# Kernel optimization log

Measured on AMD Instinct MI355X. Metric: run time of the kernel, lower is better.

The kernel has to match this reference:

```python
import jax, jax.numpy as jnp
import numpy as np


def _conv(x, w, b, stride=1):
    # NCHW conv, 3x3 kernel, padding=1
    y = jax.lax.conv_general_dilated(
        x, w, (stride, stride), [(1, 1), (1, 1)],
        dimension_numbers=("NCHW", "OIHW", "NCHW"))
    return y + b[None, :, None, None]


def setup_inputs() -> dict:
    key = jax.random.key(0)
    ks = jax.random.split(key, 13)
    s = 0.05
    d = jnp.float32
    return {
        "x": jax.random.normal(ks[0], (1, 3, 512, 512), d),
        "low0_w": jax.random.normal(ks[1], (64, 3, 3, 3), d) * s,
        "low0_b": jax.random.normal(ks[2], (64,), d) * s,
        "ll_rh_w": jax.random.normal(ks[3], (4, 61, 61, 3, 3), d) * s,
        "ll_rh_b": jax.random.normal(ks[4], (4, 61), d) * s,
        "ll_lh_w": jax.random.normal(ks[5], (4, 3, 3, 3, 3), d) * s,
        "ll_lh_b": jax.random.normal(ks[6], (4, 3), d) * s,
        "hl0_w": jax.random.normal(ks[7], (64, 61, 3, 3), d) * s,
        "hl0_b": jax.random.normal(ks[8], (64,), d) * s,
        "hl_w": jax.random.normal(ks[9], (3, 64, 64, 3, 3), d) * s,
        "hl_b": jax.random.normal(ks[10], (3, 64), d) * s,
        "lin_w": jax.random.normal(ks[11], (30, 64), d) * s,
        "lin_b": jax.random.normal(ks[12], (30,), d) * s,
    }


def reference(x, low0_w, low0_b, ll_rh_w, ll_rh_b, ll_lh_w, ll_lh_b,
              hl0_w, hl0_b, hl_w, hl_b, lin_w, lin_b):
    # ---- low-level path: 64-channel full-resolution features ----
    I = _conv(x, low0_w, low0_b)  # (b,64,H,W)
    for i in range(ll_rh_w.shape[0]):
        rh = jax.nn.relu(_conv(I[:, :61], ll_rh_w[i], ll_rh_b[i]))
        lh = jnp.tanh(_conv(I[:, 61:], ll_lh_w[i], ll_lh_b[i]))
        I = jnp.concatenate([rh, lh], axis=1)
    # ---- high-level path: predicts 30 params -> 3x10 color transform ----
    h = _conv(I[:, :61], hl0_w, hl0_b)
    for i in range(hl_w.shape[0]):
        h = jax.nn.relu(_conv(h, hl_w[i], hl_b[i], stride=2))
        h = jax.lax.reduce_window(h, -jnp.inf, jax.lax.max,
                                  (1, 1, 2, 2), (1, 1, 2, 2), "VALID")
    g = h.mean(axis=(2, 3))            # (b,64) global average pool
    Wp = g @ lin_w.T + lin_b           # (b,30)
    Wm = Wp.reshape(3, 10)             # batch=1, matches torch reshape
    # ---- vectorized Tform: per-pixel quadratic feature expansion ----
    I3 = I[:, 61:]                     # (b,3,H,W)
    r, gc, bc = I3[:, 0], I3[:, 1], I3[:, 2]
    feats = jnp.stack([r * r, r * gc, r * bc, r,
                       gc * gc, gc * bc, gc,
                       bc * bc, bc, jnp.ones_like(r)], axis=1)  # (b,10,H,W)
    return jnp.einsum("ok,bkhw->bohw", Wm, feats)  # (b,3,H,W)
```

## Files before the change

### kernel.cpp

```cpp
#include <hip/hip_runtime.h>
#include <cstdint>

typedef _Float16 half8 __attribute__((ext_vector_type(8)));
typedef float f32x4 __attribute__((ext_vector_type(4)));

#define HW_ (512*512)

__global__ __launch_bounds__(256) void wtrans_k(
    const float* __restrict__ rh_w, const float* __restrict__ hl0_w,
    const float* __restrict__ hl_w, _Float16* __restrict__ wt,
    _Float16* __restrict__ zg)
{
    if (blockIdx.x == 0 && threadIdx.x < 32) zg[threadIdx.x] = (_Float16)0.f;
    int t = blockIdx.x * 256 + threadIdx.x;
    if (t >= 8 * 4608) return;
    int layer = t / 4608;
    int r = t - layer * 4608;
    int lane = r & 63, ci = r >> 6;
    int m = ci & 3, kk = (ci >> 2) & 1, s = ci >> 3;
    int o = m * 16 + (lane & 15);
    int cb = kk * 32 + ((lane >> 4) & 3) * 8;
    const float* w; int O, CIN;
    if (layer < 4)      { w = rh_w + (size_t)layer * 61 * 61 * 9; O = 61; CIN = 61; }
    else if (layer == 4){ w = hl0_w;                              O = 64; CIN = 61; }
    else                { w = hl_w + (size_t)(layer - 5) * 64 * 64 * 9; O = 64; CIN = 64; }
    half8 v;
    #pragma unroll
    for (int j = 0; j < 8; ++j) {
        int c = cb + j;
        float f = (o < O && c < CIN) ? w[((size_t)o * CIN + c) * 9 + s] : 0.f;
        v[j] = (_Float16)f;
    }
    *(half8*)(wt + (size_t)layer * 36864 + (size_t)r * 8) = v;
}

__global__ __launch_bounds__(256)
void low0_k(const float* __restrict__ x, const float* __restrict__ w,
            const float* __restrict__ bias, _Float16* __restrict__ M,
            float* __restrict__ L)
{
    __shared__ float tile[3 * 324];
    const int tx = threadIdx.x & 15, ty = threadIdx.x >> 4;
    const int bx = blockIdx.x, by = blockIdx.y, z = blockIdx.z;
    const int ox = bx * 16 + tx, oy = by * 16 + ty;
    const int ix0 = bx * 16 - 1, iy0 = by * 16 - 1;

    for (int i = threadIdx.x; i < 3 * 324; i += 256) {
        int c = i / 324, p = i - c * 324;
        int iy = p / 18, ix = p - iy * 18;
        int gy = iy0 + iy, gx = ix0 + ix;
        float v = 0.f;
        if ((unsigned)gy < 512u && (unsigned)gx < 512u)
            v = x[(size_t)c * HW_ + (size_t)gy * 512 + gx];
        tile[i] = v;
    }
    __syncthreads();

    float p9[3][9];
    #pragma unroll
    for (int c = 0; c < 3; ++c)
        #pragma unroll
        for (int dy = 0; dy < 3; ++dy)
            #pragma unroll
            for (int dx = 0; dx < 3; ++dx)
                p9[c][dy * 3 + dx] = tile[c * 324 + (ty + dy) * 18 + tx + dx];

    float acc[16];
    #pragma unroll
    for (int o = 0; o < 16; ++o) {
        int oc = z * 16 + o;
        float a = bias[oc];
        const float* wo = w + (size_t)oc * 27;
        #pragma unroll
        for (int c = 0; c < 3; ++c)
            #pragma unroll
            for (int k = 0; k < 9; ++k)
                a = fmaf(p9[c][k], wo[c * 9 + k], a);
        acc[o] = a;
    }

    const size_t pix = (size_t)oy * 512 + ox;
    half8 h0, h1;
    #pragma unroll
    for (int o = 0; o < 8; ++o) { h0[o] = (_Float16)acc[o]; h1[o] = (_Float16)acc[8 + o]; }
    _Float16* orow = M + pix * 64 + z * 16;
    *(half8*)(orow)     = h0;
    *(half8*)(orow + 8) = h1;
    if (z == 3) {
        #pragma unroll
        for (int o = 13; o < 16; ++o)
            L[(size_t)(o - 13) * HW_ + pix] = acc[o];
    }
}

template<int O, int ACT, int DOLH>
__global__ __launch_bounds__(256, 3)
void conv_mfma_k(const _Float16* __restrict__ in, const _Float16* __restrict__ wt,
                 const float* __restrict__ bias, _Float16* __restrict__ out,
                 const float* __restrict__ L_in, const float* __restrict__ lhw,
                 const float* __restrict__ lhb, float* __restrict__ L_out,
                 const _Float16* __restrict__ zg)
{
    __shared__ _Float16 __attribute__((aligned(16))) in_t[2816 * 8];
    __shared__ float lh_t[3 * 324];
    const int tid = threadIdx.x;
    const int l = tid & 63, wv = tid >> 6;
    const int px = l & 15, g = l >> 4;
    const int bx = blockIdx.x, by = blockIdx.y;
    const int iy0 = by * 16 - 1, ix0 = bx * 16 - 1;

    #pragma unroll
    for (int k = 0; k < 11; ++k) {
        int i = tid + (k << 8);
        int p = i >> 3, jl = i & 7;
        int iy = p / 18, ix = p - iy * 18;
        int gy = iy0 + iy, gx = ix0 + ix;
        int j = jl ^ (p & 7);
        const _Float16* src =
            (p < 324 && (unsigned)gy < 512u && (unsigned)gx < 512u)
                ? in + ((size_t)gy * 512 + gx) * 64 + j * 8 : zg;
        __builtin_amdgcn_global_load_lds(
            (const __attribute__((address_space(1))) void*)src,
            (__attribute__((address_space(3))) void*)(in_t + (size_t)(tid - l + (k << 8)) * 8),
            16, 0, 0);
    }
    if (DOLH) {
        for (int i = tid; i < 3 * 324; i += 256) {
            int c = i / 324, p = i - c * 324;
            int iy = p / 18, ix = p - iy * 18;
            int gy = iy0 + iy, gx = ix0 + ix;
            float v = 0.f;
            if ((unsigned)gy < 512u && (unsigned)gx < 512u)
                v = L_in[(size_t)c * HW_ + (size_t)gy * 512 + gx];
            lh_t[i] = v;
        }
    }
    __syncthreads();

    float bs[4][4];
    #pragma unroll
    for (int m = 0; m < 4; ++m)
        #pragma unroll
        for (int r = 0; r < 4; ++r) {
            int o = m * 16 + g * 4 + r;
            bs[m][r] = (o < O) ? bias[o] : 0.f;
        }

    f32x4 acc[4][4];
    #pragma unroll
    for (int m = 0; m < 4; ++m)
        #pragma unroll
        for (int f = 0; f < 4; ++f) acc[m][f] = (f32x4){0.f, 0.f, 0.f, 0.f};

    const _Float16* wb = wt + (size_t)l * 8;
    half8 aA[8], aB[8];
    #pragma unroll
    for (int q = 0; q < 8; ++q) aA[q] = *(const half8*)(wb + q * 512);

    #pragma unroll
    for (int s = 0; s < 9; ++s) {
        asm volatile("" ::: "memory");
        const half8* ac = (s & 1) ? aB : aA;
        half8*       an = (s & 1) ? aA : aB;
        if (s < 8) {
            #pragma unroll
            for (int q = 0; q < 8; ++q)
                an[q] = *(const half8*)(wb + ((s + 1) * 8 + q) * 512);
        }
        const int dy = s / 3, dx = s - dy * 3;
        #pragma unroll
        for (int f = 0; f < 4; ++f) {
            int ipix = (4 * wv + f + dy) * 18 + px + dx;
            int rb = ipix * 64, sw = (ipix & 7) << 3;
            #pragma unroll
            for (int kk = 0; kk < 2; ++kk) {
                half8 b = *(const half8*)&in_t[rb + ((kk * 32 + g * 8) ^ sw)];
                #pragma unroll
                for (int m = 0; m < 4; ++m)
                    acc[m][f] = __builtin_amdgcn_mfma_f32_16x16x32_f16(
                        ac[kk * 4 + m], b, acc[m][f], 0, 0, 0);
            }
        }
    }

    if (DOLH) {
        const int tx = tid & 15, ty = tid >> 4;
        const size_t pix = (size_t)(by * 16 + ty) * 512 + bx * 16 + tx;
        #pragma unroll
        for (int oc = 0; oc < 3; ++oc) {
            float a = lhb[oc];
            #pragma unroll
            for (int c = 0; c < 3; ++c)
                #pragma unroll
                for (int t9 = 0; t9 < 9; ++t9) {
                    int dy = t9 / 3, dx = t9 - dy * 3;
                    a = fmaf(lh_t[c * 324 + (ty + dy) * 18 + tx + dx],
                             lhw[(oc * 3 + c) * 9 + t9], a);
                }
            L_out[(size_t)oc * HW_ + pix] = tanhf(a);
        }
    }

    __syncthreads();
    #pragma unroll
    for (int f = 0; f < 4; ++f) {
        const int p = (4 * wv + f) * 16 + px;
        const int sw = p & 7;
        #pragma unroll
        for (int m = 0; m < 4; ++m) {
            union { _Float16 h[4]; uint2 u; } pk;
            #pragma unroll
            for (int r = 0; r < 4; ++r) {
                int o = m * 16 + g * 4 + r;
                float v = acc[m][f][r] + bs[m][r];
                if (ACT) v = fmaxf(v, 0.f);
                pk.h[r] = (o < O) ? (_Float16)v : (_Float16)0.f;
            }
            int chunk = (m * 2 + (g >> 1)) ^ sw;
            *(uint2*)&in_t[p * 64 + chunk * 8 + (g & 1) * 4] = pk.u;
        }
    }
    __syncthreads();
    #pragma unroll
    for (int k = 0; k < 8; ++k) {
        int q = (k << 8) + tid;
        int p = q >> 3, jc = q & 7;
        half8 v = *(const half8*)&in_t[p * 64 + ((jc ^ (p & 7)) * 8)];
        int row = p >> 4, col = p & 15;
        _Float16* dst = out + (((size_t)(by * 16 + row) * 512) + bx * 16 + col) * 64 + jc * 8;
        *(half8*)dst = v;
    }
}

template<int FP32OUT>
__global__ __launch_bounds__(256, 3)
void conv_s2_pool_k(const _Float16* __restrict__ in, int Hin,
                    const _Float16* __restrict__ wt,
                    const float* __restrict__ bias, void* __restrict__ outv,
                    const _Float16* __restrict__ zg)
{
    const int Hp = Hin >> 2;
    __shared__ _Float16 __attribute__((aligned(16))) in_t[2560 * 8];
    const int tid = threadIdx.x;
    const int l = tid & 63, wv = tid >> 6;
    const int n = l & 15, g = l >> 4;
    const int bx = blockIdx.x, by = blockIdx.y;
    const int iy0 = by * 16 - 1, ix0 = bx * 16 - 1;

    #pragma unroll
    for (int k = 0; k < 10; ++k) {
        int i = tid + (k << 8);
        int p = i >> 3, jl = i & 7;
        int iy = p / 17, ix = p - iy * 17;
        int gy = iy0 + iy, gx = ix0 + ix;
        int j = jl ^ (p & 7);
        const _Float16* src =
            (p < 289 && (unsigned)gy < (unsigned)Hin && (unsigned)gx < (unsigned)Hin)
                ? in + ((size_t)gy * Hin + gx) * 64 + j * 8 : zg;
        __builtin_amdgcn_global_load_lds(
            (const __attribute__((address_space(1))) void*)src,
            (__attribute__((address_space(3))) void*)(in_t + (size_t)(tid - l + (k << 8)) * 8),
            16, 0, 0);
    }
    __syncthreads();

    float bs[4];
    #pragma unroll
    for (int r = 0; r < 4; ++r) bs[r] = bias[wv * 16 + g * 4 + r];

    f32x4 acc[4];
    #pragma unroll
    for (int f = 0; f < 4; ++f) acc[f] = (f32x4){0.f, 0.f, 0.f, 0.f};

    const int py_lo = n >> 3, pxc = n & 7;
    #pragma unroll
    for (int s = 0; s < 9; ++s) {
        const int dy = s / 3, dx = s - dy * 3;
        half8 a[2];
        #pragma unroll
        for (int kk = 0; kk < 2; ++kk)
            a[kk] = *(const half8*)(wt + (size_t)(s * 8 + kk * 4 + wv) * 512 + l * 8);
        #pragma unroll
        for (int f = 0; f < 4; ++f) {
            int py = 2 * f + py_lo;
            int ipix = (2 * py + dy) * 17 + 2 * pxc + dx;
            int rb = ipix * 64, sw = (ipix & 7) << 3;
            #pragma unroll
            for (int kk = 0; kk < 2; ++kk) {
                half8 b = *(const half8*)&in_t[rb + ((kk * 32 + g * 8) ^ sw)];
                acc[f] = __builtin_amdgcn_mfma_f32_16x16x32_f16(a[kk], b, acc[f], 0, 0, 0);
            }
        }
    }

    #pragma unroll
    for (int f = 0; f < 4; ++f)
        #pragma unroll
        for (int r = 0; r < 4; ++r) {
            float v = fmaxf(acc[f][r] + bs[r], 0.f);
            v = fmaxf(v, __shfl_xor(v, 1));
            v = fmaxf(v, __shfl_xor(v, 8));
            if ((l & 9) == 0) {
                int o = wv * 16 + g * 4 + r;
                size_t pp = ((size_t)(by * 4 + f) * Hp + bx * 4 + (n >> 1)) * 64 + o;
                if (FP32OUT) ((float*)outv)[pp] = v;
                else         ((_Float16*)outv)[pp] = (_Float16)v;
            }
        }
}

__global__ void meanlin_k(const float* __restrict__ h,
                          const float* __restrict__ lw,
                          const float* __restrict__ lb,
                          float* __restrict__ wm)
{
    __shared__ float g[64];
    int t = threadIdx.x;
    if (t < 64) {
        float s = 0.f;
        for (int p = 0; p < 64; ++p) s += h[p * 64 + t];
        g[t] = s * (1.f / 64.f);
    }
    __syncthreads();
    if (t < 30) {
        float s = lb[t];
        for (int c = 0; c < 64; ++c) s = fmaf(g[c], lw[t * 64 + c], s);
        wm[t] = s;
    }
}

__global__ __launch_bounds__(256)
void final_k(const float* __restrict__ I3, const float* __restrict__ wm,
             float* __restrict__ out)
{
    __shared__ float W[30];
    if (threadIdx.x < 30) W[threadIdx.x] = wm[threadIdx.x];
    __syncthreads();
    const int HW = 512 * 512;
    for (int i = blockIdx.x * blockDim.x + threadIdx.x; i < HW;
         i += gridDim.x * blockDim.x) {
        float r = I3[i], g = I3[HW + i], b = I3[2 * HW + i];
        float f[10] = { r * r, r * g, r * b, r, g * g, g * b, g, b * b, b, 1.f };
        #pragma unroll
        for (int o = 0; o < 3; ++o) {
            float s = 0.f;
            #pragma unroll
            for (int k = 0; k < 10; ++k) s = fmaf(W[o * 10 + k], f[k], s);
            out[(size_t)o * HW + i] = s;
        }
    }
}

extern "C" void kernel_launch(void* const* d_in, const int* in_sizes, int n_in,
                              void* d_out, int out_size, void* d_ws, size_t ws_size,
                              hipStream_t stream)
{
    const float* x      = (const float*)d_in[0];
    const float* low0_w = (const float*)d_in[1];
    const float* low0_b = (const float*)d_in[2];
    const float* rh_w   = (const float*)d_in[3];
    const float* rh_b   = (const float*)d_in[4];
    const float* lh_w   = (const float*)d_in[5];
    const float* lh_b   = (const float*)d_in[6];
    const float* hl0_w  = (const float*)d_in[7];
    const float* hl0_b  = (const float*)d_in[8];
    const float* hl_w   = (const float*)d_in[9];
    const float* hl_b   = (const float*)d_in[10];
    const float* lin_w  = (const float*)d_in[11];
    const float* lin_b  = (const float*)d_in[12];
    float* out = (float*)d_out;

    const size_t HW = 512 * 512;
    _Float16* M0 = (_Float16*)d_ws;
    _Float16* M1 = M0 + (size_t)64 * HW;
    _Float16* P0 = M1 + (size_t)64 * HW;
    _Float16* P1 = P0 + (size_t)16384 * 64;
    _Float16* WT = P1 + (size_t)1024 * 64;
    _Float16* ZG = WT + (size_t)8 * 36864;
    float*    P2 = (float*)(ZG + 32);
    float*    L0 = P2 + 64 * 64;
    float*    L1 = L0 + (size_t)3 * HW;
    float*    WM = L1 + (size_t)3 * HW;

    dim3 blk(256);
    dim3 g512(32, 32, 1);

    wtrans_k<<<dim3(144), blk, 0, stream>>>(rh_w, hl0_w, hl_w, WT, ZG);

    low0_k<<<dim3(32, 32, 4), blk, 0, stream>>>(x, low0_w, low0_b, M0, L0);

    _Float16* cur = M0; _Float16* nxt = M1;
    float* Lc = L0; float* Ln = L1;
    for (int i = 0; i < 4; ++i) {
        conv_mfma_k<61, 1, 1><<<g512, blk, 0, stream>>>(
            cur, WT + (size_t)i * 36864, rh_b + i * 61, nxt,
            Lc, lh_w + (size_t)i * 81, lh_b + i * 3, Ln, ZG);
        _Float16* t = cur; cur = nxt; nxt = t;
        float* tl = Lc; Lc = Ln; Ln = tl;
    }

    conv_mfma_k<64, 0, 0><<<g512, blk, 0, stream>>>(
        cur, WT + (size_t)4 * 36864, hl0_b, nxt,
        nullptr, nullptr, nullptr, nullptr, ZG);

    conv_s2_pool_k<0><<<dim3(32, 32), blk, 0, stream>>>(
        nxt, 512, WT + (size_t)5 * 36864, hl_b, (void*)P0, ZG);
    conv_s2_pool_k<0><<<dim3(8, 8), blk, 0, stream>>>(
        P0, 128, WT + (size_t)6 * 36864, hl_b + 64, (void*)P1, ZG);
    conv_s2_pool_k<1><<<dim3(2, 2), blk, 0, stream>>>(
        P1, 32, WT + (size_t)7 * 36864, hl_b + 128, (void*)P2, ZG);

    meanlin_k<<<dim3(1), dim3(64), 0, stream>>>(P2, lin_w, lin_b, WM);

    final_k<<<dim3(2048), blk, 0, stream>>>(Lc, WM, out);
}
```

Measured before the change: 259.7 us.

## Stage conv weights through double-buffered LDS via async global_load_lds

```diff
diff --git a/kernel.cpp b/kernel.cpp
--- a/kernel.cpp
+++ b/kernel.cpp
@@ -94,15 +94,16 @@
 }
 
 template<int O, int ACT, int DOLH>
-__global__ __launch_bounds__(256, 3)
+__global__ __launch_bounds__(256, 2)
 void conv_mfma_k(const _Float16* __restrict__ in, const _Float16* __restrict__ wt,
                  const float* __restrict__ bias, _Float16* __restrict__ out,
                  const float* __restrict__ L_in, const float* __restrict__ lhw,
                  const float* __restrict__ lhb, float* __restrict__ L_out,
                  const _Float16* __restrict__ zg)
 {
-    __shared__ _Float16 __attribute__((aligned(16))) in_t[2816 * 8];
-    __shared__ float lh_t[3 * 324];
+    __shared__ _Float16 __attribute__((aligned(16))) in_t[2592 * 8];
+    __shared__ _Float16 __attribute__((aligned(16))) wbuf[2][4096];
+    __shared__ float lh_t[DOLH ? 3 * 324 : 4];
     const int tid = threadIdx.x;
     const int l = tid & 63, wv = tid >> 6;
     const int px = l & 15, g = l >> 4;
@@ -112,16 +113,25 @@
     #pragma unroll
     for (int k = 0; k < 11; ++k) {
         int i = tid + (k << 8);
-        int p = i >> 3, jl = i & 7;
-        int iy = p / 18, ix = p - iy * 18;
-        int gy = iy0 + iy, gx = ix0 + ix;
-        int j = jl ^ (p & 7);
-        const _Float16* src =
-            (p < 324 && (unsigned)gy < 512u && (unsigned)gx < 512u)
+        if (i < 2592) {
+            int p = i >> 3, jl = i & 7;
+            int iy = p / 18, ix = p - iy * 18;
+            int gy = iy0 + iy, gx = ix0 + ix;
+            int j = jl ^ (p & 7);
+            const _Float16* src = ((unsigned)gy < 512u && (unsigned)gx < 512u)
                 ? in + ((size_t)gy * 512 + gx) * 64 + j * 8 : zg;
+            __builtin_amdgcn_global_load_lds(
+                (const __attribute__((address_space(1))) void*)src,
+                (__attribute__((address_space(3))) void*)(in_t + (size_t)(i - l) * 8),
+                16, 0, 0);
+        }
+    }
+    #pragma unroll
+    for (int it = 0; it < 2; ++it) {
+        int ci = (it << 8) + tid;
         __builtin_amdgcn_global_load_lds(
-            (const __attribute__((address_space(1))) void*)src,
-            (__attribute__((address_space(3))) void*)(in_t + (size_t)(tid - l + (k << 8)) * 8),
+            (const __attribute__((address_space(1))) void*)(wt + ci * 8),
+            (__attribute__((address_space(3))) void*)(wbuf[0] + (size_t)(ci - l) * 8),
             16, 0, 0);
     }
     if (DOLH) {
@@ -152,21 +162,24 @@
         #pragma unroll
         for (int f = 0; f < 4; ++f) acc[m][f] = (f32x4){0.f, 0.f, 0.f, 0.f};
 
-    const _Float16* wb = wt + (size_t)l * 8;
-    half8 aA[8], aB[8];
-    #pragma unroll
-    for (int q = 0; q < 8; ++q) aA[q] = *(const half8*)(wb + q * 512);
-
     #pragma unroll
     for (int s = 0; s < 9; ++s) {
-        asm volatile("" ::: "memory");
-        const half8* ac = (s & 1) ? aB : aA;
-        half8*       an = (s & 1) ? aA : aB;
         if (s < 8) {
             #pragma unroll
-            for (int q = 0; q < 8; ++q)
-                an[q] = *(const half8*)(wb + ((s + 1) * 8 + q) * 512);
-        }
+            for (int it = 0; it < 2; ++it) {
+                int ci = (it << 8) + tid;
+                __builtin_amdgcn_global_load_lds(
+                    (const __attribute__((address_space(1))) void*)(wt + ((s + 1) << 12) + ci * 8),
+                    (__attribute__((address_space(3))) void*)(wbuf[(s + 1) & 1] + (size_t)(ci - l) * 8),
+                    16, 0, 0);
+            }
+        }
+        const _Float16* wb = wbuf[s & 1];
+        half8 a[8];
+        #pragma unroll
+        for (int q = 0; q < 8; ++q)
+            a[q] = *(const half8*)(wb + (q << 9) + l * 8);
+
         const int dy = s / 3, dx = s - dy * 3;
         #pragma unroll
         for (int f = 0; f < 4; ++f) {
@@ -178,9 +191,10 @@
                 #pragma unroll
                 for (int m = 0; m < 4; ++m)
                     acc[m][f] = __builtin_amdgcn_mfma_f32_16x16x32_f16(
-                        ac[kk * 4 + m], b, acc[m][f], 0, 0, 0);
-            }
-        }
+                        a[kk * 4 + m], b, acc[m][f], 0, 0, 0);
+            }
+        }
+        __syncthreads();
     }
 
     if (DOLH) {
@@ -201,7 +215,6 @@
         }
     }
 
-    __syncthreads();
     #pragma unroll
     for (int f = 0; f < 4; ++f) {
         const int p = (4 * wv + f) * 16 + px;
@@ -240,7 +253,8 @@
                     const _Float16* __restrict__ zg)
 {
     const int Hp = Hin >> 2;
-    __shared__ _Float16 __attribute__((aligned(16))) in_t[2560 * 8];
+    __shared__ _Float16 __attribute__((aligned(16))) in_t[2312 * 8];
+    __shared__ _Float16 __attribute__((aligned(16))) wbuf[2][4096];
     const int tid = threadIdx.x;
     const int l = tid & 63, wv = tid >> 6;
     const int n = l & 15, g = l >> 4;
@@ -250,16 +264,26 @@
     #pragma unroll
     for (int k = 0; k < 10; ++k) {
         int i = tid + (k << 8);
-        int p = i >> 3, jl = i & 7;
-        int iy = p / 17, ix = p - iy * 17;
-        int gy = iy0 + iy, gx = ix0 + ix;
-        int j = jl ^ (p & 7);
-        const _Float16* src =
-            (p < 289 && (unsigned)gy < (unsigned)Hin && (unsigned)gx < (unsigned)Hin)
-                ? in + ((size_t)gy * Hin + gx) * 64 + j * 8 : zg;
+        if (i < 2312) {
+            int p = i >> 3, jl = i & 7;
+            int iy = p / 17, ix = p - iy * 17;
+            int gy = iy0 + iy, gx = ix0 + ix;
+            int j = jl ^ (p & 7);
+            const _Float16* src =
+                ((unsigned)gy < (unsigned)Hin && (unsigned)gx < (unsigned)Hin)
+                    ? in + ((size_t)gy * Hin + gx) * 64 + j * 8 : zg;
+            __builtin_amdgcn_global_load_lds(
+                (const __attribute__((address_space(1))) void*)src,
+                (__attribute__((address_space(3))) void*)(in_t + (size_t)(i - l) * 8),
+                16, 0, 0);
+        }
+    }
+    #pragma unroll
+    for (int it = 0; it < 2; ++it) {
+        int ci = (it << 8) + tid;
         __builtin_amdgcn_global_load_lds(
-            (const __attribute__((address_space(1))) void*)src,
-            (__attribute__((address_space(3))) void*)(in_t + (size_t)(tid - l + (k << 8)) * 8),
+            (const __attribute__((address_space(1))) void*)(wt + ci * 8),
+            (__attribute__((address_space(3))) void*)(wbuf[0] + (size_t)(ci - l) * 8),
             16, 0, 0);
     }
     __syncthreads();
@@ -275,11 +299,23 @@
     const int py_lo = n >> 3, pxc = n & 7;
     #pragma unroll
     for (int s = 0; s < 9; ++s) {
+        if (s < 8) {
+            #pragma unroll
+            for (int it = 0; it < 2; ++it) {
+                int ci = (it << 8) + tid;
+                __builtin_amdgcn_global_load_lds(
+                    (const __attribute__((address_space(1))) void*)(wt + ((s + 1) << 12) + ci * 8),
+                    (__attribute__((address_space(3))) void*)(wbuf[(s + 1) & 1] + (size_t)(ci - l) * 8),
+                    16, 0, 0);
+            }
+        }
+        const _Float16* wb = wbuf[s & 1];
+        half8 a[2];
+        #pragma unroll
+        for (int kk = 0; kk < 2; ++kk)
+            a[kk] = *(const half8*)(wb + ((kk * 4 + wv) << 9) + l * 8);
+
         const int dy = s / 3, dx = s - dy * 3;
-        half8 a[2];
-        #pragma unroll
-        for (int kk = 0; kk < 2; ++kk)
-            a[kk] = *(const half8*)(wt + (size_t)(s * 8 + kk * 4 + wv) * 512 + l * 8);
         #pragma unroll
         for (int f = 0; f < 4; ++f) {
             int py = 2 * f + py_lo;
@@ -291,6 +327,7 @@
                 acc[f] = __builtin_amdgcn_mfma_f32_16x16x32_f16(a[kk], b, acc[f], 0, 0, 0);
             }
         }
+        __syncthreads();
     }
 
     #pragma unroll
```

After: 228.9 us. -11.9%, faster.

## Stage conv weights through double-buffered LDS and raise occupancy target

Applied to the files above, without the earlier changes.

```diff
diff --git a/kernel.cpp b/kernel.cpp
--- a/kernel.cpp
+++ b/kernel.cpp
@@ -94,15 +94,15 @@
 }
 
 template<int O, int ACT, int DOLH>
-__global__ __launch_bounds__(256, 3)
+__global__ __launch_bounds__(256, 4)
 void conv_mfma_k(const _Float16* __restrict__ in, const _Float16* __restrict__ wt,
                  const float* __restrict__ bias, _Float16* __restrict__ out,
                  const float* __restrict__ L_in, const float* __restrict__ lhw,
                  const float* __restrict__ lhb, float* __restrict__ L_out,
                  const _Float16* __restrict__ zg)
 {
-    __shared__ _Float16 __attribute__((aligned(16))) in_t[2816 * 8];
-    __shared__ float lh_t[3 * 324];
+    __shared__ _Float16 __attribute__((aligned(16))) in_t[2592 * 8];
+    __shared__ _Float16 __attribute__((aligned(16))) wbuf[2][2048];
     const int tid = threadIdx.x;
     const int l = tid & 63, wv = tid >> 6;
     const int px = l & 15, g = l >> 4;
@@ -112,30 +112,58 @@
     #pragma unroll
     for (int k = 0; k < 11; ++k) {
         int i = tid + (k << 8);
-        int p = i >> 3, jl = i & 7;
-        int iy = p / 18, ix = p - iy * 18;
-        int gy = iy0 + iy, gx = ix0 + ix;
-        int j = jl ^ (p & 7);
-        const _Float16* src =
-            (p < 324 && (unsigned)gy < 512u && (unsigned)gx < 512u)
-                ? in + ((size_t)gy * 512 + gx) * 64 + j * 8 : zg;
-        __builtin_amdgcn_global_load_lds(
-            (const __attribute__((address_space(1))) void*)src,
-            (__attribute__((address_space(3))) void*)(in_t + (size_t)(tid - l + (k << 8)) * 8),
-            16, 0, 0);
-    }
-    if (DOLH) {
-        for (int i = tid; i < 3 * 324; i += 256) {
-            int c = i / 324, p = i - c * 324;
+        if (i < 2592) {
+            int p = i >> 3, jl = i & 7;
             int iy = p / 18, ix = p - iy * 18;
             int gy = iy0 + iy, gx = ix0 + ix;
-            float v = 0.f;
-            if ((unsigned)gy < 512u && (unsigned)gx < 512u)
-                v = L_in[(size_t)c * HW_ + (size_t)gy * 512 + gx];
-            lh_t[i] = v;
-        }
-    }
-    __syncthreads();
+            int j = jl ^ (p & 7);
+            const _Float16* src = ((unsigned)gy < 512u && (unsigned)gx < 512u)
+                ? in + ((size_t)gy * 512 + gx) * 64 + j * 8 : zg;
+            __builtin_amdgcn_global_load_lds(
+                (const __attribute__((address_space(1))) void*)src,
+                (__attribute__((address_space(3))) void*)(in_t + (size_t)(i - l) * 8),
+                16, 0, 0);
+        }
+    }
+    __builtin_amdgcn_global_load_lds(
+        (const __attribute__((address_space(1))) void*)(wt + tid * 8),
+        (__attribute__((address_space(3))) void*)(wbuf[0] + (size_t)(tid - l) * 8),
+        16, 0, 0);
+    __syncthreads();
+
+    f32x4 acc[4][4];
+    #pragma unroll
+    for (int m = 0; m < 4; ++m)
+        #pragma unroll
+        for (int f = 0; f < 4; ++f) acc[m][f] = (f32x4){0.f, 0.f, 0.f, 0.f};
+
+    #pragma unroll
+    for (int ph = 0; ph < 18; ++ph) {
+        if (ph < 17) {
+            __builtin_amdgcn_global_load_lds(
+                (const __attribute__((address_space(1))) void*)(wt + ((ph + 1) << 11) + tid * 8),
+                (__attribute__((address_space(3))) void*)(wbuf[(ph + 1) & 1] + (size_t)(tid - l) * 8),
+                16, 0, 0);
+        }
+        const int s = ph >> 1, kk = ph & 1;
+        const int dy = s / 3, dx = s - dy * 3;
+        const _Float16* wb = wbuf[ph & 1];
+        half8 a[4];
+        #pragma unroll
+        for (int m = 0; m < 4; ++m)
+            a[m] = *(const half8*)(wb + (m << 9) + l * 8);
+        #pragma unroll
+        for (int f = 0; f < 4; ++f) {
+            int ipix = (4 * wv + f + dy) * 18 + px + dx;
+            int rb = ipix * 64, sw = (ipix & 7) << 3;
+            half8 b = *(const half8*)&in_t[rb + ((kk * 32 + g * 8) ^ sw)];
+            #pragma unroll
+            for (int m = 0; m < 4; ++m)
+                acc[m][f] = __builtin_amdgcn_mfma_f32_16x16x32_f16(
+                    a[m], b, acc[m][f], 0, 0, 0);
+        }
+        __syncthreads();
+    }
 
     float bs[4][4];
     #pragma unroll
@@ -146,62 +174,6 @@
             bs[m][r] = (o < O) ? bias[o] : 0.f;
         }
 
-    f32x4 acc[4][4];
-    #pragma unroll
-    for (int m = 0; m < 4; ++m)
-        #pragma unroll
-        for (int f = 0; f < 4; ++f) acc[m][f] = (f32x4){0.f, 0.f, 0.f, 0.f};
-
-    const _Float16* wb = wt + (size_t)l * 8;
-    half8 aA[8], aB[8];
-    #pragma unroll
-    for (int q = 0; q < 8; ++q) aA[q] = *(const half8*)(wb + q * 512);
-
-    #pragma unroll
-    for (int s = 0; s < 9; ++s) {
-        asm volatile("" ::: "memory");
-        const half8* ac = (s & 1) ? aB : aA;
-        half8*       an = (s & 1) ? aA : aB;
-        if (s < 8) {
-            #pragma unroll
-            for (int q = 0; q < 8; ++q)
-                an[q] = *(const half8*)(wb + ((s + 1) * 8 + q) * 512);
-        }
-        const int dy = s / 3, dx = s - dy * 3;
-        #pragma unroll
-        for (int f = 0; f < 4; ++f) {
-            int ipix = (4 * wv + f + dy) * 18 + px + dx;
-            int rb = ipix * 64, sw = (ipix & 7) << 3;
-            #pragma unroll
-            for (int kk = 0; kk < 2; ++kk) {
-                half8 b = *(const half8*)&in_t[rb + ((kk * 32 + g * 8) ^ sw)];
-                #pragma unroll
-                for (int m = 0; m < 4; ++m)
-                    acc[m][f] = __builtin_amdgcn_mfma_f32_16x16x32_f16(
-                        ac[kk * 4 + m], b, acc[m][f], 0, 0, 0);
-            }
-        }
-    }
-
-    if (DOLH) {
-        const int tx = tid & 15, ty = tid >> 4;
-        const size_t pix = (size_t)(by * 16 + ty) * 512 + bx * 16 + tx;
-        #pragma unroll
-        for (int oc = 0; oc < 3; ++oc) {
-            float a = lhb[oc];
-            #pragma unroll
-            for (int c = 0; c < 3; ++c)
-                #pragma unroll
-                for (int t9 = 0; t9 < 9; ++t9) {
-                    int dy = t9 / 3, dx = t9 - dy * 3;
-                    a = fmaf(lh_t[c * 324 + (ty + dy) * 18 + tx + dx],
-                             lhw[(oc * 3 + c) * 9 + t9], a);
-                }
-            L_out[(size_t)oc * HW_ + pix] = tanhf(a);
-        }
-    }
-
-    __syncthreads();
     #pragma unroll
     for (int f = 0; f < 4; ++f) {
         const int p = (4 * wv + f) * 16 + px;
@@ -230,17 +202,41 @@
         _Float16* dst = out + (((size_t)(by * 16 + row) * 512) + bx * 16 + col) * 64 + jc * 8;
         *(half8*)dst = v;
     }
+
+    if (DOLH) {
+        const int tx = tid & 15, ty = tid >> 4;
+        const int oy = by * 16 + ty, ox = bx * 16 + tx;
+        float pv[27];
+        #pragma unroll
+        for (int c = 0; c < 3; ++c)
+            #pragma unroll
+            for (int d2 = 0; d2 < 9; ++d2) {
+                int gy = oy + d2 / 3 - 1, gx = ox + d2 % 3 - 1;
+                pv[c * 9 + d2] = ((unsigned)gy < 512u && (unsigned)gx < 512u)
+                    ? L_in[(size_t)c * HW_ + (size_t)gy * 512 + gx] : 0.f;
+            }
+        const size_t pix = (size_t)oy * 512 + ox;
+        #pragma unroll
+        for (int oc = 0; oc < 3; ++oc) {
+            float a = lhb[oc];
+            #pragma unroll
+            for (int k = 0; k < 27; ++k)
+                a = fmaf(pv[k], lhw[oc * 27 + k], a);
+            L_out[(size_t)oc * HW_ + pix] = tanhf(a);
+        }
+    }
 }
 
 template<int FP32OUT>
-__global__ __launch_bounds__(256, 3)
+__global__ __launch_bounds__(256, 4)
 void conv_s2_pool_k(const _Float16* __restrict__ in, int Hin,
                     const _Float16* __restrict__ wt,
                     const float* __restrict__ bias, void* __restrict__ outv,
                     const _Float16* __restrict__ zg)
 {
     const int Hp = Hin >> 2;
-    __shared__ _Float16 __attribute__((aligned(16))) in_t[2560 * 8];
+    __shared__ _Float16 __attribute__((aligned(16))) in_t[2312 * 8];
+    __shared__ _Float16 __attribute__((aligned(16))) wbuf[2][2048];
     const int tid = threadIdx.x;
     const int l = tid & 63, wv = tid >> 6;
     const int n = l & 15, g = l >> 4;
@@ -250,23 +246,25 @@
     #pragma unroll
     for (int k = 0; k < 10; ++k) {
         int i = tid + (k << 8);
-        int p = i >> 3, jl = i & 7;
-        int iy = p / 17, ix = p - iy * 17;
-        int gy = iy0 + iy, gx = ix0 + ix;
-        int j = jl ^ (p & 7);
-        const _Float16* src =
-            (p < 289 && (unsigned)gy < (unsigned)Hin && (unsigned)gx < (unsigned)Hin)
-                ? in + ((size_t)gy * Hin + gx) * 64 + j * 8 : zg;
-        __builtin_amdgcn_global_load_lds(
-            (const __attribute__((address_space(1))) void*)src,
-            (__attribute__((address_space(3))) void*)(in_t + (size_t)(tid - l + (k << 8)) * 8),
-            16, 0, 0);
-    }
-    __syncthreads();
-
-    float bs[4];
-    #pragma unroll
-    for (int r = 0; r < 4; ++r) bs[r] = bias[wv * 16 + g * 4 + r];
+        if (i < 2312) {
+            int p = i >> 3, jl = i & 7;
+            int iy = p / 17, ix = p - iy * 17;
+            int gy = iy0 + iy, gx = ix0 + ix;
+            int j = jl ^ (p & 7);
+            const _Float16* src =
+                ((unsigned)gy < (unsigned)Hin && (unsigned)gx < (unsigned)Hin)
+                    ? in + ((size_t)gy * Hin + gx) * 64 + j * 8 : zg;
+            __builtin_amdgcn_global_load_lds(
+                (const __attribute__((address_space(1))) void*)src,
+                (__attribute__((address_space(3))) void*)(in_t + (size_t)(i - l) * 8),
+                16, 0, 0);
+        }
+    }
+    __builtin_amdgcn_global_load_lds(
+        (const __attribute__((address_space(1))) void*)(wt + tid * 8),
+        (__attribute__((address_space(3))) void*)(wbuf[0] + (size_t)(tid - l) * 8),
+        16, 0, 0);
+    __syncthreads();
 
     f32x4 acc[4];
     #pragma unroll
@@ -274,24 +272,30 @@
 
     const int py_lo = n >> 3, pxc = n & 7;
     #pragma unroll
-    for (int s = 0; s < 9; ++s) {
+    for (int ph = 0; ph < 18; ++ph) {
+        if (ph < 17) {
+            __builtin_amdgcn_global_load_lds(
+                (const __attribute__((address_space(1))) void*)(wt + ((ph + 1) << 11) + tid * 8),
+                (__attribute__((address_space(3))) void*)(wbuf[(ph + 1) & 1] + (size_t)(tid - l) * 8),
+                16, 0, 0);
+        }
+        const int s = ph >> 1, kk = ph & 1;
         const int dy = s / 3, dx = s - dy * 3;
-        half8 a[2];
-        #pragma unroll
-        for (int kk = 0; kk < 2; ++kk)
-            a[kk] = *(const half8*)(wt + (size_t)(s * 8 + kk * 4 + wv) * 512 + l * 8);
+        half8 a = *(const half8*)(wbuf[ph & 1] + (wv << 9) + l * 8);
         #pragma unroll
         for (int f = 0; f < 4; ++f) {
             int py = 2 * f + py_lo;
             int ipix = (2 * py + dy) * 17 + 2 * pxc + dx;
             int rb = ipix * 64, sw = (ipix & 7) << 3;
-            #pragma unroll
-            for (int kk = 0; kk < 2; ++kk) {
-                half8 b = *(const half8*)&in_t[rb + ((kk * 32 + g * 8) ^ sw)];
-                acc[f] = __builtin_amdgcn_mfma_f32_16x16x32_f16(a[kk], b, acc[f], 0, 0, 0);
-            }
-        }
-    }
+            half8 b = *(const half8*)&in_t[rb + ((kk * 32 + g * 8) ^ sw)];
+            acc[f] = __builtin_amdgcn_mfma_f32_16x16x32_f16(a, b, acc[f], 0, 0, 0);
+        }
+        __syncthreads();
+    }
+
+    float bs[4];
+    #pragma unroll
+    for (int r = 0; r < 4; ++r) bs[r] = bias[wv * 16 + g * 4 + r];
 
     #pragma unroll
     for (int f = 0; f < 4; ++f)
```

Measured after the change: 251.3 us. 3.3% less time.
